# Kernel tuning notes

Hardware: AMD Instinct MI355X
Metric: run time of the kernel (lower is better)

Reference implementation:

```python
import jax, jax.numpy as jnp
import numpy as np
from jax import lax

B, C, H, W = 8, 256, 128, 128
RED = 4  # SE reduction


def setup_inputs() -> dict:
    key = jax.random.key(0)
    ks = jax.random.split(key, 7)
    s = 0.05
    return {
        "x": jax.random.normal(ks[0], (B, C, H, W), dtype=jnp.float32),
        "w_deform": jax.random.normal(ks[1], (C, C, 3, 3), dtype=jnp.float32) * s,
        "b_deform": jax.random.normal(ks[2], (C,), dtype=jnp.float32) * s,
        "w_se1": jax.random.normal(ks[3], (C // RED, C), dtype=jnp.float32) * s,
        "b_se1": jax.random.normal(ks[4], (C // RED,), dtype=jnp.float32) * s,
        "w_se2": jax.random.normal(ks[5], (C, C // RED), dtype=jnp.float32) * s,
        "b_se2": jax.random.normal(ks[6], (C,), dtype=jnp.float32) * s,
    }


def reference(x, w_deform, b_deform, w_se1, b_se1, w_se2, b_se2):
    # DeformConv2d with the all-zero offset tensor used in forward(): bilinear
    # sampling at integer taps == standard 3x3 conv, padding=1, zero-padded borders.
    y = lax.conv_general_dilated(
        x, w_deform,
        window_strides=(1, 1),
        padding=((1, 1), (1, 1)),
        dimension_numbers=("NCHW", "OIHW", "NCHW"),
    ) + b_deform[None, :, None, None]  # [B, C, H, W]

    # SE: global average pool -> 1x1 conv -> ReLU -> 1x1 conv -> sigmoid
    p = y.mean(axis=(2, 3))                                   # [B, C]
    h = jax.nn.relu(p @ w_se1.T + b_se1)                      # [B, C//RED]
    scale = jax.nn.sigmoid(h @ w_se2.T + b_se2)               # [B, C]
    return y * scale[:, :, None, None]
```

## Files before the change

kernel.cpp:

```cpp
#include <hip/hip_runtime.h>
#include <hip/hip_bf16.h>

#define BB 8
#define CC 256
#define HH 128
#define WW 128

typedef __attribute__((ext_vector_type(8))) short bf16x8;
typedef __attribute__((ext_vector_type(4))) float f32x4;

static __device__ __forceinline__ unsigned short f2bf(float f) {
  unsigned int u = __builtin_bit_cast(unsigned int, f);
  u += 0x7fffu + ((u >> 16) & 1u);
  return (unsigned short)(u >> 16);
}

static __device__ __forceinline__ void async16(const void* g, void* l) {
#if __has_builtin(__builtin_amdgcn_global_load_lds)
  __builtin_amdgcn_global_load_lds(
      (__attribute__((address_space(1))) void*)(unsigned long long)(g),
      (__attribute__((address_space(3))) void*)(unsigned int)(unsigned long long)(l),
      16, 0, 0);
#else
  *(bf16x8*)l = *(const bf16x8*)g;
#endif
}

__global__ __launch_bounds__(256) void k_convert_w(const float* __restrict__ w,
                                                   unsigned short* __restrict__ Wt,
                                                   float* __restrict__ sums) {
  __shared__ unsigned short lw[8 * 2304];
  const int t = threadIdx.x;
  const int co0 = blockIdx.x << 3;
  for (int z = blockIdx.x * 256 + t; z < 18432; z += 8192) sums[z] = 0.f;
  const float* src = w + co0 * 2304;
  for (int k = t; k < 18432; k += 256) lw[k] = f2bf(src[k]);
  __syncthreads();
  for (int g = t; g < 18432; g += 256) {
    const int tap = g >> 11, rem = g & 2047;
    const int o = rem >> 6, rem2 = rem & 63;
    const int cl = rem2 >> 3, e = rem2 & 7;
    Wt[(((tap << 5) + o) << 11) + ((co0 + cl) << 3) + e] =
        lw[cl * 2304 + ((o << 3) + e) * 9 + tap];
  }
}

__global__ __launch_bounds__(256) void k_transpose_x(const float* __restrict__ x,
                                                     unsigned short* __restrict__ Xc,
                                                     float* __restrict__ sums) {
  __shared__ float tile[64][65];
  const int t = threadIdx.x;
  const int bz = blockIdx.z;
  const int b = bz >> 7, h = bz & 127;
  const int c0 = blockIdx.y << 6, w0 = blockIdx.x << 6;
  const float* xp = x + (((b * CC) * HH) + h) * WW;
#pragma unroll
  for (int i = 0; i < 4; ++i) {
    int idx = t + (i << 8);
    int cr = idx >> 4, wq = idx & 15;
    float4 v = *(const float4*)(xp + (c0 + cr) * (HH * WW) + w0 + (wq << 2));
    tile[cr][(wq << 2) + 0] = v.x;
    tile[cr][(wq << 2) + 1] = v.y;
    tile[cr][(wq << 2) + 2] = v.z;
    tile[cr][(wq << 2) + 3] = v.w;
  }
  __syncthreads();
  const int ob = c0 >> 3;
#pragma unroll
  for (int i = 0; i < 2; ++i) {
    int g = t + (i << 8);
    int o = g >> 6, wr = g & 63;
    bf16x8 v;
#pragma unroll
    for (int e = 0; e < 8; ++e) v[e] = (short)f2bf(tile[(o << 3) + e][wr]);
    *(bf16x8*)(Xc + ((((b << 7) + h) * 32) + ob + o) * 1024 + (w0 + wr) * 8) = v;
  }
  {
    const int c = t >> 2, seg = t & 3;
    float s = 0.f;
#pragma unroll
    for (int k = 0; k < 16; ++k) s += tile[c][(seg << 4) + k];
    s += __shfl_xor(s, 1);
    s += __shfl_xor(s, 2);
    const int ci = b * CC + c0 + c;
    if (seg == 0) {
      atomicAdd(&sums[ci], s);
      if (h == 0)   atomicAdd(&sums[2048 + ci], s);
      if (h == 127) atomicAdd(&sums[4096 + ci], s);
      if (w0 == 0) {
        atomicAdd(&sums[6144 + ci], tile[c][0]);
        if (h == 0)   atomicAdd(&sums[10240 + ci], tile[c][0]);
        if (h == 127) atomicAdd(&sums[14336 + ci], tile[c][0]);
      }
    }
    if (seg == 3 && w0 == 64) {
      atomicAdd(&sums[8192 + ci], tile[c][63]);
      if (h == 0)   atomicAdd(&sums[12288 + ci], tile[c][63]);
      if (h == 127) atomicAdd(&sums[16384 + ci], tile[c][63]);
    }
  }
}

__global__ __launch_bounds__(256) void k_pool2(const float* __restrict__ w,
                                               const float* __restrict__ bd,
                                               const float* __restrict__ sums,
                                               float* __restrict__ p_buf) {
  __shared__ float ts[2304];
  const int b = blockIdx.y, t = threadIdx.x;
  const int lane = t & 63, wid = t >> 6;
  {
    const int ci = (b << 8) + t;
    const float S  = sums[ci];
    const float R0 = sums[2048 + ci], R1 = sums[4096 + ci];
    const float C0 = sums[6144 + ci], C1 = sums[8192 + ci];
    const float x00 = sums[10240 + ci], x0W = sums[12288 + ci];
    const float xH0 = sums[14336 + ci], xHW = sums[16384 + ci];
    const float er[3] = {R1, 0.f, R0};
    const float ec[3] = {C1, 0.f, C0};
    const float cor[9] = {xHW, 0.f, xH0, 0.f, 0.f, 0.f, x0W, 0.f, x00};
#pragma unroll
    for (int kh = 0; kh < 3; ++kh)
#pragma unroll
      for (int kw = 0; kw < 3; ++kw)
        ts[t * 9 + kh * 3 + kw] = S - er[kh] - ec[kw] + cor[kh * 3 + kw];
  }
  __syncthreads();
  float4 tv[9];
#pragma unroll
  for (int q = 0; q < 9; ++q) tv[q] = *(const float4*)&ts[(q * 64 + lane) * 4];
  const int co = (blockIdx.x << 3) + (wid << 1);
#pragma unroll
  for (int c2 = 0; c2 < 2; ++c2) {
    const float4* wr = (const float4*)(w + (co + c2) * 2304) + lane;
    float s = 0.f;
#pragma unroll
    for (int q = 0; q < 9; ++q) {
      float4 wv = wr[q * 64];
      s += wv.x * tv[q].x + wv.y * tv[q].y + wv.z * tv[q].z + wv.w * tv[q].w;
    }
    s += __shfl_xor(s, 1);  s += __shfl_xor(s, 2);  s += __shfl_xor(s, 4);
    s += __shfl_xor(s, 8);  s += __shfl_xor(s, 16); s += __shfl_xor(s, 32);
    if (lane == 0) p_buf[(b << 8) + co + c2] = bd[co + c2] + s * (1.0f / 16384.0f);
  }
}

__global__ __launch_bounds__(256) void k_se2(const float* __restrict__ p_buf,
                                             const float* __restrict__ w1,
                                             const float* __restrict__ b1,
                                             const float* __restrict__ w2,
                                             const float* __restrict__ b2,
                                             float* __restrict__ scale) {
  __shared__ float p[CC];
  __shared__ float h1[64];
  const int b = blockIdx.x, t = threadIdx.x;
  const int lane = t & 63, wid = t >> 6;
  p[t] = p_buf[(b << 8) + t];
  __syncthreads();
  {
    const float4 pv = *(const float4*)&p[lane << 2];
#pragma unroll
    for (int i = 0; i < 16; ++i) {
      const int r = (wid << 4) + i;
      float4 wv = ((const float4*)(w1 + (r << 8)))[lane];
      float s = wv.x * pv.x + wv.y * pv.y + wv.z * pv.z + wv.w * pv.w;
      s += __shfl_xor(s, 1);  s += __shfl_xor(s, 2);  s += __shfl_xor(s, 4);
      s += __shfl_xor(s, 8);  s += __shfl_xor(s, 16); s += __shfl_xor(s, 32);
      if (lane == 0) {
        float v = b1[r] + s;
        h1[r] = v > 0.f ? v : 0.f;
      }
    }
  }
  __syncthreads();
  {
    float s = b2[t];
    const float* wr = w2 + (t << 6);
#pragma unroll
    for (int k = 0; k < 64; ++k) s += wr[k] * h1[k];
    scale[(b << 8) + t] = 1.0f / (1.0f + expf(-s));
  }
}

__global__ __launch_bounds__(256, 2) void k_conv(
    const unsigned short* __restrict__ Xc, const unsigned short* __restrict__ Wt,
    const float* __restrict__ bias, const float* __restrict__ scale,
    float* __restrict__ out) {
  extern __shared__ __align__(16) unsigned short Xs[];
  const int t = threadIdx.x;
  const int lin = (blockIdx.y << 1) | blockIdx.x;
  const int Wk = ((lin & 7) << 7) | (lin >> 3);
  const int m0 = (Wk & 1) << 7;
  const int bhp = Wk >> 1;
  const int b = bhp >> 6;
  const int h0 = (bhp & 63) << 1;
  const int lane = t & 63, wid = t >> 6;
  const int wave_m = (wid & 1) << 6, wave_n = (wid >> 1) << 6;
  const int n0 = lane & 15, quad = lane >> 4;
  const int part = wid & 1, rsel = wid >> 1;

  bf16x8 z8 = {0, 0, 0, 0, 0, 0, 0, 0};
  if (t < 64) {
    int bi = t >> 5, rem = t & 31;
    int dh = rem >> 3, rem2 = rem & 7, q = rem2 >> 1, side = rem2 & 1;
    *(bf16x8*)&Xs[bi * 16640 + dh * 4160 + q * 1040 + (side ? 1032 : 0)] = z8;
  }
  if (h0 == 0 || h0 == 126) {
    const int dhz = (h0 == 0) ? 0 : 3;
    for (int g = t; g < 1040; g += 256) {
      int bi = g >= 520, gg = g - bi * 520;
      *(bf16x8*)&Xs[bi * 16640 + dhz * 4160 + gg * 8] = z8;
    }
  }

  auto stage = [&](int cb8, int bi) {
    const int ob = cb8 << 2;
#pragma unroll
    for (int r = 0; r < 8; ++r) {
      const int rr = (r << 1) | rsel;
      const int dh = rr >> 2, q = rr & 3;
      const int hh = h0 - 1 + dh;
      if (hh >= 0 && hh < HH) {
        const unsigned short* gp =
            Xc + ((((b << 7) + hh) * 32 + ob + q) << 10) + (part << 9) + (lane << 3);
        unsigned short* lp =
            &Xs[bi * 16640 + dh * 4160 + q * 1040 + 8 + (part << 9) + (lane << 3)];
        async16(gp, lp);
      }
    }
  };

  f32x4 acc[2][4][4];
  f32x4 zero4 = {0.f, 0.f, 0.f, 0.f};
#pragma unroll
  for (int r = 0; r < 2; ++r)
#pragma unroll
    for (int i = 0; i < 4; ++i)
#pragma unroll
      for (int j = 0; j < 4; ++j) acc[r][i][j] = zero4;

  stage(0, 0);
  __syncthreads();

  for (int cb8 = 0; cb8 < 8; ++cb8) {
    const int cur = cb8 & 1;
    if (cb8 < 7) stage(cb8 + 1, cur ^ 1);
    const unsigned short* wb =
        Wt + ((((cb8 << 2) + quad) << 8) + m0 + wave_m + n0) * 8;
    const unsigned short* xb = &Xs[cur * 16640 + quad * 1040 + (wave_n + n0) * 8];

    bf16x8 af[3][4], bg[2][4];
#pragma unroll
    for (int i = 0; i < 4; ++i) af[0][i] = *(const bf16x8*)(wb + 0 * 65536 + i * 128);
#pragma unroll
    for (int i = 0; i < 4; ++i) af[1][i] = *(const bf16x8*)(wb + 3 * 65536 + i * 128);
#pragma unroll
    for (int j = 0; j < 4; ++j) bg[0][j] = *(const bf16x8*)(xb + (j << 4) * 8);

#pragma unroll
    for (int kw = 0; kw < 3; ++kw) {
#pragma unroll
      for (int dh = 0; dh < 4; ++dh) {
        const int s = (kw << 2) + dh;
        if (s < 11) {
          const int sn = s + 1, kwn = sn >> 2, dhn = sn & 3;
#pragma unroll
          for (int j = 0; j < 4; ++j)
            bg[sn & 1][j] =
                *(const bf16x8*)(xb + dhn * 4160 + (((j << 4) + kwn)) * 8);
        }
        if (dh >= 1) {
          const int p1 = kw * 3 + dh - 1;
#pragma unroll
          for (int i = 0; i < 4; ++i)
#pragma unroll
            for (int j = 0; j < 4; ++j)
              acc[1][i][j] = __builtin_amdgcn_mfma_f32_16x16x32_bf16(
                  af[p1 % 3][i], bg[s & 1][j], acc[1][i][j], 0, 0, 0);
        }
        if (dh <= 2) {
          const int p0 = kw * 3 + dh;
#pragma unroll
          for (int i = 0; i < 4; ++i)
#pragma unroll
            for (int j = 0; j < 4; ++j)
              acc[0][i][j] = __builtin_amdgcn_mfma_f32_16x16x32_bf16(
                  af[p0 % 3][i], bg[s & 1][j], acc[0][i][j], 0, 0, 0);
        }
        if (s >= 1 && s <= 7) {
          const int pn = s + 1;
          const int tapn = (pn % 3) * 3 + pn / 3;
#pragma unroll
          for (int i = 0; i < 4; ++i)
            af[pn % 3][i] = *(const bf16x8*)(wb + tapn * 65536 + i * 128);
        }
      }
    }
    __syncthreads();
  }

#pragma unroll
  for (int i = 0; i < 4; ++i) {
    const int mrow = m0 + wave_m + (i << 4) + (quad << 2);
    float bs[4], ss[4];
#pragma unroll
    for (int r4 = 0; r4 < 4; ++r4) {
      bs[r4] = bias[mrow + r4];
      ss[r4] = scale[(b << 8) + mrow + r4];
    }
#pragma unroll
    for (int r = 0; r < 2; ++r)
#pragma unroll
      for (int j = 0; j < 4; ++j) {
        const int wcol = wave_n + (j << 4) + n0;
        float* op = out + ((((b << 8) + mrow) * HH) + h0 + r) * WW + wcol;
#pragma unroll
        for (int r4 = 0; r4 < 4; ++r4)
          op[r4 * (HH * WW)] = (acc[r][i][j][r4] + bs[r4]) * ss[r4];
      }
  }
}

extern "C" void kernel_launch(void* const* d_in, const int* in_sizes, int n_in,
                              void* d_out, int out_size, void* d_ws, size_t ws_size,
                              hipStream_t stream) {
  const float* x  = (const float*)d_in[0];
  const float* wd = (const float*)d_in[1];
  const float* bd = (const float*)d_in[2];
  const float* w1 = (const float*)d_in[3];
  const float* b1 = (const float*)d_in[4];
  const float* w2 = (const float*)d_in[5];
  const float* b2 = (const float*)d_in[6];
  float* out = (float*)d_out;

  char* ws = (char*)d_ws;
  unsigned short* Xc = (unsigned short*)ws;
  unsigned short* Wt = (unsigned short*)(ws + 67108864);
  float* sums  = (float*)(ws + 68288512);
  float* p_buf = (float*)(ws + 68362240);
  float* scale = (float*)(ws + 68370432);

  (void)hipFuncSetAttribute((const void*)k_conv,
                            hipFuncAttributeMaxDynamicSharedMemorySize, 66560);

  k_convert_w<<<dim3(32), dim3(256), 0, stream>>>(wd, Wt, sums);
  k_transpose_x<<<dim3(2, 4, 1024), dim3(256), 0, stream>>>(x, Xc, sums);
  k_pool2<<<dim3(32, 8), dim3(256), 0, stream>>>(wd, bd, sums, p_buf);
  k_se2<<<dim3(8), dim3(256), 0, stream>>>(p_buf, w1, b1, w2, b2, scale);
  k_conv<<<dim3(2, 512), dim3(256), 66560, stream>>>(Xc, Wt, bd, scale, out);
}
```

Before: 382.9 us.

## Replace atomic pooling sums with per-row partials and raise MFMA wave priority

The transpose kernel now handles a full 128-wide row per block. Instead of atomically accumulating channel and border sums, it writes per-(b,h,c) row partials, plus the first and last columns, into scratch space borrowed from the output buffer. The pool kernel then reduces these partials over h, which removes both the atomics and the zeroing pass. It also wraps the MFMA section of the conv loop in s_setprio to favour matrix issue over loads. The cost is that each pool thread does a serial 128-step reduction, and the design relies on the output buffer being free until the conv writes it.

Result: no change. 381.4 us (-0.4%).

```diff
diff --git a/kernel.cpp b/kernel.cpp
--- a/kernel.cpp
+++ b/kernel.cpp
@@ -27,12 +27,10 @@
 }
 
 __global__ __launch_bounds__(256) void k_convert_w(const float* __restrict__ w,
-                                                   unsigned short* __restrict__ Wt,
-                                                   float* __restrict__ sums) {
+                                                   unsigned short* __restrict__ Wt) {
   __shared__ unsigned short lw[8 * 2304];
   const int t = threadIdx.x;
   const int co0 = blockIdx.x << 3;
-  for (int z = blockIdx.x * 256 + t; z < 18432; z += 8192) sums[z] = 0.f;
   const float* src = w + co0 * 2304;
   for (int k = t; k < 18432; k += 256) lw[k] = f2bf(src[k]);
   __syncthreads();
@@ -47,18 +45,20 @@
 
 __global__ __launch_bounds__(256) void k_transpose_x(const float* __restrict__ x,
                                                      unsigned short* __restrict__ Xc,
-                                                     float* __restrict__ sums) {
-  __shared__ float tile[64][65];
+                                                     float* __restrict__ pS,
+                                                     float* __restrict__ pC0,
+                                                     float* __restrict__ pC1) {
+  __shared__ float tile[64][130];
   const int t = threadIdx.x;
-  const int bz = blockIdx.z;
-  const int b = bz >> 7, h = bz & 127;
-  const int c0 = blockIdx.y << 6, w0 = blockIdx.x << 6;
-  const float* xp = x + (((b * CC) * HH) + h) * WW;
-#pragma unroll
-  for (int i = 0; i < 4; ++i) {
+  const int bh = blockIdx.y;
+  const int b = bh >> 7;
+  const int c0 = blockIdx.x << 6;
+  const float* xp = x + ((b * CC) * HH + (bh & 127)) * WW;
+#pragma unroll
+  for (int i = 0; i < 8; ++i) {
     int idx = t + (i << 8);
-    int cr = idx >> 4, wq = idx & 15;
-    float4 v = *(const float4*)(xp + (c0 + cr) * (HH * WW) + w0 + (wq << 2));
+    int cr = idx >> 5, wq = idx & 31;
+    float4 v = *(const float4*)(xp + (c0 + cr) * (HH * WW) + (wq << 2));
     tile[cr][(wq << 2) + 0] = v.x;
     tile[cr][(wq << 2) + 1] = v.y;
     tile[cr][(wq << 2) + 2] = v.z;
@@ -67,54 +67,52 @@
   __syncthreads();
   const int ob = c0 >> 3;
 #pragma unroll
-  for (int i = 0; i < 2; ++i) {
+  for (int i = 0; i < 4; ++i) {
     int g = t + (i << 8);
-    int o = g >> 6, wr = g & 63;
+    int o = g >> 7, wr = g & 127;
     bf16x8 v;
 #pragma unroll
     for (int e = 0; e < 8; ++e) v[e] = (short)f2bf(tile[(o << 3) + e][wr]);
-    *(bf16x8*)(Xc + ((((b << 7) + h) * 32) + ob + o) * 1024 + (w0 + wr) * 8) = v;
+    *(bf16x8*)(Xc + ((bh * 32) + ob + o) * 1024 + wr * 8) = v;
   }
   {
     const int c = t >> 2, seg = t & 3;
     float s = 0.f;
 #pragma unroll
-    for (int k = 0; k < 16; ++k) s += tile[c][(seg << 4) + k];
+    for (int k = 0; k < 32; ++k)
+      s += tile[c][(seg << 5) + ((k + (seg << 3)) & 31)];
     s += __shfl_xor(s, 1);
     s += __shfl_xor(s, 2);
-    const int ci = b * CC + c0 + c;
     if (seg == 0) {
-      atomicAdd(&sums[ci], s);
-      if (h == 0)   atomicAdd(&sums[2048 + ci], s);
-      if (h == 127) atomicAdd(&sums[4096 + ci], s);
-      if (w0 == 0) {
-        atomicAdd(&sums[6144 + ci], tile[c][0]);
-        if (h == 0)   atomicAdd(&sums[10240 + ci], tile[c][0]);
-        if (h == 127) atomicAdd(&sums[14336 + ci], tile[c][0]);
-      }
-    }
-    if (seg == 3 && w0 == 64) {
-      atomicAdd(&sums[8192 + ci], tile[c][63]);
-      if (h == 0)   atomicAdd(&sums[12288 + ci], tile[c][63]);
-      if (h == 127) atomicAdd(&sums[16384 + ci], tile[c][63]);
+      const int idx = (bh << 8) + c0 + c;
+      pS[idx]  = s;
+      pC0[idx] = tile[c][0];
+      pC1[idx] = tile[c][127];
     }
   }
 }
 
 __global__ __launch_bounds__(256) void k_pool2(const float* __restrict__ w,
                                                const float* __restrict__ bd,
-                                               const float* __restrict__ sums,
+                                               const float* __restrict__ pS,
+                                               const float* __restrict__ pC0,
+                                               const float* __restrict__ pC1,
                                                float* __restrict__ p_buf) {
   __shared__ float ts[2304];
   const int b = blockIdx.y, t = threadIdx.x;
   const int lane = t & 63, wid = t >> 6;
   {
-    const int ci = (b << 8) + t;
-    const float S  = sums[ci];
-    const float R0 = sums[2048 + ci], R1 = sums[4096 + ci];
-    const float C0 = sums[6144 + ci], C1 = sums[8192 + ci];
-    const float x00 = sums[10240 + ci], x0W = sums[12288 + ci];
-    const float xH0 = sums[14336 + ci], xHW = sums[16384 + ci];
+    const int base = (b << 15) + t;
+    float S = 0.f, C0 = 0.f, C1 = 0.f;
+#pragma unroll 4
+    for (int h = 0; h < 128; ++h) {
+      S  += pS [base + (h << 8)];
+      C0 += pC0[base + (h << 8)];
+      C1 += pC1[base + (h << 8)];
+    }
+    const float R0 = pS[base],  R1 = pS[base + (127 << 8)];
+    const float x00 = pC0[base], xH0 = pC0[base + (127 << 8)];
+    const float x0W = pC1[base], xHW = pC1[base + (127 << 8)];
     const float er[3] = {R1, 0.f, R0};
     const float ec[3] = {C1, 0.f, C0};
     const float cor[9] = {xHW, 0.f, xH0, 0.f, 0.f, 0.f, x0W, 0.f, x00};
@@ -268,6 +266,7 @@
             bg[sn & 1][j] =
                 *(const bf16x8*)(xb + dhn * 4160 + (((j << 4) + kwn)) * 8);
         }
+        __builtin_amdgcn_s_setprio(1);
         if (dh >= 1) {
           const int p1 = kw * 3 + dh - 1;
 #pragma unroll
@@ -286,6 +285,7 @@
               acc[0][i][j] = __builtin_amdgcn_mfma_f32_16x16x32_bf16(
                   af[p0 % 3][i], bg[s & 1][j], acc[0][i][j], 0, 0, 0);
         }
+        __builtin_amdgcn_s_setprio(0);
         if (s >= 1 && s <= 7) {
           const int pn = s + 1;
           const int tapn = (pn % 3) * 3 + pn / 3;
@@ -335,16 +335,19 @@
   char* ws = (char*)d_ws;
   unsigned short* Xc = (unsigned short*)ws;
   unsigned short* Wt = (unsigned short*)(ws + 67108864);
-  float* sums  = (float*)(ws + 68288512);
   float* p_buf = (float*)(ws + 68362240);
   float* scale = (float*)(ws + 68370432);
 
+  float* pS  = out;
+  float* pC0 = out + 262144;
+  float* pC1 = out + 524288;
+
   (void)hipFuncSetAttribute((const void*)k_conv,
                             hipFuncAttributeMaxDynamicSharedMemorySize, 66560);
 
-  k_convert_w<<<dim3(32), dim3(256), 0, stream>>>(wd, Wt, sums);
-  k_transpose_x<<<dim3(2, 4, 1024), dim3(256), 0, stream>>>(x, Xc, sums);
-  k_pool2<<<dim3(32, 8), dim3(256), 0, stream>>>(wd, bd, sums, p_buf);
+  k_convert_w<<<dim3(32), dim3(256), 0, stream>>>(wd, Wt);
+  k_transpose_x<<<dim3(4, 1024), dim3(256), 0, stream>>>(x, Xc, pS, pC0, pC1);
+  k_pool2<<<dim3(32, 8), dim3(256), 0, stream>>>(wd, bd, pS, pC0, pC1, p_buf);
   k_se2<<<dim3(8), dim3(256), 0, stream>>>(p_buf, w1, b1, w2, b2, scale);
   k_conv<<<dim3(2, 512), dim3(256), 66560, stream>>>(Xc, Wt, bd, scale, out);
 }
```
